# Kernel tuning notes

Measured on AMD Instinct MI355X. Metric: run time of the kernel, lower is better.

## Reference

```python
import jax, jax.numpy as jnp
import numpy as np

D, H, L, P, NQ, B, DFF = 256, 8, 4, 4, 900, 4, 1024
SHAPES = [(128, 128), (64, 64), (32, 32), (16, 16)]
S = sum(h * w for h, w in SHAPES)  # 21760
HD = D // H


def setup_inputs() -> dict:
    key = jax.random.key(0)
    ks = iter(jax.random.split(key, 32))
    r = lambda sh, s=1.0: jax.random.normal(next(ks), sh, jnp.float32) * s
    return dict(
        tgt=r((B, NQ, D)),
        query_pos=r((B, NQ, D)),
        reference_points=jax.random.uniform(next(ks), (B, NQ, L, 2), jnp.float32),
        memory=r((B, S, D)),
        in_proj_w=r((D, 3 * D), 0.02), in_proj_b=jnp.zeros(3 * D, jnp.float32),
        out_proj_w=r((D, D), 0.02), out_proj_b=jnp.zeros(D, jnp.float32),
        ln1_g=jnp.ones(D, jnp.float32), ln1_b=jnp.zeros(D, jnp.float32),
        ln2_g=jnp.ones(D, jnp.float32), ln2_b=jnp.zeros(D, jnp.float32),
        ln3_g=jnp.ones(D, jnp.float32), ln3_b=jnp.zeros(D, jnp.float32),
        vproj_w=r((D, D), 0.02), vproj_b=jnp.zeros(D, jnp.float32),
        off_w=r((D, H * L * P * 2), 0.02), off_b=r((H * L * P * 2,), 0.5),
        aw_w=r((D, H * L * P), 0.02), aw_b=jnp.zeros(H * L * P, jnp.float32),
        oproj_w=r((D, D), 0.02), oproj_b=jnp.zeros(D, jnp.float32),
        lin1_w=r((D, DFF), 0.02), lin1_b=jnp.zeros(DFF, jnp.float32),
        lin2_w=r((DFF, D), 0.02), lin2_b=jnp.zeros(D, jnp.float32),
        spatial_shapes=np.array(SHAPES, np.int32),
        mem_mask=jnp.zeros((B, S), bool),
    )


def _ln(x, g, b):
    m = jnp.mean(x, -1, keepdims=True)
    v = jnp.mean((x - m) ** 2, -1, keepdims=True)
    return (x - m) * jax.lax.rsqrt(v + 1e-5) * g + b


def reference(tgt, query_pos, reference_points, memory,
              in_proj_w, in_proj_b, out_proj_w, out_proj_b,
              ln1_g, ln1_b, ln2_g, ln2_b, ln3_g, ln3_b,
              vproj_w, vproj_b, off_w, off_b, aw_w, aw_b, oproj_w, oproj_b,
              lin1_w, lin1_b, lin2_w, lin2_b, spatial_shapes, mem_mask):
    shapes = np.asarray(spatial_shapes)  # static level shapes

    # ---- self attention (nn.MultiheadAttention, q=k=tgt+pos, v=tgt) ----
    qp = tgt + query_pos
    q = qp @ in_proj_w[:, :D] + in_proj_b[:D]
    k = qp @ in_proj_w[:, D:2 * D] + in_proj_b[D:2 * D]
    v = tgt @ in_proj_w[:, 2 * D:] + in_proj_b[2 * D:]
    split = lambda x: x.reshape(B, NQ, H, HD).transpose(0, 2, 1, 3)
    qh, kh, vh = split(q), split(k), split(v)
    att = jax.nn.softmax(jnp.einsum('bhqd,bhkd->bhqk', qh, kh) / np.sqrt(HD).astype(np.float32), -1)
    sa = jnp.einsum('bhqk,bhkd->bhqd', att, vh).transpose(0, 2, 1, 3).reshape(B, NQ, D)
    tgt = _ln(tgt + sa @ out_proj_w + out_proj_b, ln2_g, ln2_b)

    # ---- MSDeformAttn cross attention ----
    query = tgt + query_pos
    value = memory @ vproj_w + vproj_b
    value = jnp.where(mem_mask[..., None], 0.0, value).reshape(B, S, H, HD)
    off = (query @ off_w + off_b).reshape(B, NQ, H, L, P, 2)
    aw = jax.nn.softmax((query @ aw_w + aw_b).reshape(B, NQ, H, L * P), -1).reshape(B, NQ, H, L, P)
    # offset normalizer is (W_l, H_l)
    normalizer = jnp.stack([jnp.asarray(shapes[:, 1]), jnp.asarray(shapes[:, 0])], -1).astype(jnp.float32)
    loc = reference_points[:, :, None, :, None, :] + off / normalizer[None, None, None, :, None, :]

    acc = jnp.zeros((B, NQ, H, HD), tgt.dtype)
    start = 0
    bidx = jnp.arange(B)[:, None, None, None]
    hidx = jnp.arange(H)[None, None, :, None]
    for l in range(L):
        Hl, Wl = int(shapes[l, 0]), int(shapes[l, 1])
        vf = value[:, start:start + Hl * Wl]  # [B, Hl*Wl, H, HD]
        # grid_sample align_corners=False, zero padding: pixel = loc*size - 0.5
        x = loc[:, :, :, l, :, 0] * Wl - 0.5  # [B,NQ,H,P]
        y = loc[:, :, :, l, :, 1] * Hl - 0.5
        x0 = jnp.floor(x); y0 = jnp.floor(y)
        wx = x - x0; wy = y - y0
        x0i = x0.astype(jnp.int32); y0i = y0.astype(jnp.int32)

        def gather(xi, yi):
            valid = (xi >= 0) & (xi < Wl) & (yi >= 0) & (yi < Hl)
            idx = jnp.clip(yi, 0, Hl - 1) * Wl + jnp.clip(xi, 0, Wl - 1)
            g = vf[bidx, idx, hidx]  # [B,NQ,H,P,HD]
            return jnp.where(valid[..., None], g, 0.0)

        samp = (gather(x0i, y0i) * ((1 - wx) * (1 - wy))[..., None]
                + gather(x0i + 1, y0i) * (wx * (1 - wy))[..., None]
                + gather(x0i, y0i + 1) * ((1 - wx) * wy)[..., None]
                + gather(x0i + 1, y0i + 1) * (wx * wy)[..., None])
        acc = acc + (samp * aw[:, :, :, l, :, None]).sum(3)
        start += Hl * Wl

    ca = acc.reshape(B, NQ, D) @ oproj_w + oproj_b
    tgt = _ln(tgt + ca, ln1_g, ln1_b)

    # ---- FFN ----
    ff = jax.nn.relu(tgt @ lin1_w + lin1_b) @ lin2_w + lin2_b
    return _ln(tgt + ff, ln3_g, ln3_b)
```

## Files before the change

### kernel.cpp

```cpp
#include <hip/hip_runtime.h>
#include <hip/hip_bf16.h>

typedef __attribute__((ext_vector_type(8))) short bf16x8;
typedef __attribute__((ext_vector_type(4))) short bf16x4;
typedef __attribute__((ext_vector_type(4))) float f32x4;

#define DEV static __device__ __forceinline__

constexpr int Bc = 4, NQc = 900, Hc = 8, Sc = 21760;
constexpr int M1 = Bc * NQc;
constexpr int NQT = (NQc + 63) / 64;
constexpr int QT16 = (NQc + 15) / 16;

DEV short f2bf(float f) {
  union { __hip_bfloat16 h; short s; } u;
  u.h = __float2bfloat16(f);
  return u.s;
}
DEV float bf2f(short s) {
  union { short s; __hip_bfloat16 h; } u;
  u.s = s;
  return __bfloat162float(u.h);
}

DEV void pack_body(const float* W, short* Wt, int K, int N, int t) {
  int n = t % N;
  int k4 = (t / N) * 4;
  bf16x4 o;
  o[0] = f2bf(W[(size_t)(k4 + 0) * N + n]);
  o[1] = f2bf(W[(size_t)(k4 + 1) * N + n]);
  o[2] = f2bf(W[(size_t)(k4 + 2) * N + n]);
  o[3] = f2bf(W[(size_t)(k4 + 3) * N + n]);
  *(bf16x4*)&Wt[((size_t)(k4 >> 5) * N + n) * 32 + (k4 & 31)] = o;
}

__global__ __launch_bounds__(256) void pack_all_k(
    const float* w0, short* t0, const float* w1, short* t1,
    const float* w2, short* t2, const float* w3, short* t3,
    const float* w4, short* t4, const float* w5, short* t5) {
  int t = blockIdx.x * 256 + threadIdx.x;
  if (t < 49152) pack_body(w0, t0, 256, 768, t);
  else if (t < 65536) pack_body(w1, t1, 256, 256, t - 49152);
  else if (t < 81920) pack_body(w2, t2, 256, 256, t - 65536);
  else if (t < 98304) pack_body(w3, t3, 256, 256, t - 81920);
  else if (t < 163840) pack_body(w4, t4, 256, 1024, t - 98304);
  else pack_body(w5, t5, 1024, 256, t - 163840);
}

template <int MODE, int ACT, int MT>
__global__ __launch_bounds__(256) void gemmv_k(
    const float* __restrict__ A, const float* __restrict__ A2,
    const short* __restrict__ Wt, const float* __restrict__ bias,
    void* __restrict__ Cv, float* __restrict__ C2, int M, int N, int K,
    const unsigned char* __restrict__ rowmask, const float* __restrict__ g,
    const float* __restrict__ beta, const float* __restrict__ resid,
    const float* __restrict__ qpos, float* __restrict__ out2) {
  constexpr int IT = MT / 16;
  __shared__ short As[MT * 40];
  __shared__ short Ws[256 * 40];
  const int nb = N >> 8;
  const int mb = blockIdx.x / nb, bn = blockIdx.x - mb * nb;
  const int tid = threadIdx.x;
  const int lane = tid & 63, wave = tid >> 6;
  const int l16 = lane & 15, quad = lane >> 4;
  const int sr = (MT == 64) ? (tid >> 2) : (tid >> 3);
  const int sk = (MT == 64) ? ((tid & 3) * 8) : ((tid & 7) * 4);
  const int arow = mb * MT + sr;
  const bool aval = arow < M;
  const bool useA2 = (MODE == 2) ? (bn < 2) : (A2 != nullptr);
  const float* ap = A + (size_t)arow * K + sk;
  const float* ap2 = (A2 ? A2 : A) + (size_t)arow * K + sk;
  const short* wp = Wt + (size_t)(bn * 256 + tid) * 32;
  const size_t wstep = (size_t)N * 32;
  const int KT = K >> 5;

  f32x4 acc[IT][4] = {};
  float4 pa0[2] = {}, pa1[2] = {};
  bf16x8 pw[2][4];

  auto loadA = [&](int s, int it) {
    if (aval) {
      const float* p = ap + it * 32;
      pa0[s] = *(const float4*)p;
      if constexpr (MT == 64) pa1[s] = *(const float4*)(p + 4);
      if (useA2) {
        const float* p2 = ap2 + it * 32;
        float4 q0 = *(const float4*)p2;
        pa0[s].x += q0.x; pa0[s].y += q0.y; pa0[s].z += q0.z; pa0[s].w += q0.w;
        if constexpr (MT == 64) {
          float4 q1 = *(const float4*)(p2 + 4);
          pa1[s].x += q1.x; pa1[s].y += q1.y; pa1[s].z += q1.z; pa1[s].w += q1.w;
        }
      }
    }
  };
  auto loadW = [&](int s, int it) {
    const short* p = wp + (size_t)it * wstep;
    pw[s][0] = *(const bf16x8*)(p + 0);
    pw[s][1] = *(const bf16x8*)(p + 8);
    pw[s][2] = *(const bf16x8*)(p + 16);
    pw[s][3] = *(const bf16x8*)(p + 24);
  };
  auto stage = [&](int s) {
    if constexpr (MT == 64) {
      bf16x8 t;
      t[0] = f2bf(pa0[s].x); t[1] = f2bf(pa0[s].y); t[2] = f2bf(pa0[s].z); t[3] = f2bf(pa0[s].w);
      t[4] = f2bf(pa1[s].x); t[5] = f2bf(pa1[s].y); t[6] = f2bf(pa1[s].z); t[7] = f2bf(pa1[s].w);
      *(bf16x8*)&As[sr * 40 + sk] = t;
    } else {
      bf16x4 t;
      t[0] = f2bf(pa0[s].x); t[1] = f2bf(pa0[s].y); t[2] = f2bf(pa0[s].z); t[3] = f2bf(pa0[s].w);
      *(bf16x4*)&As[sr * 40 + sk] = t;
    }
    short* wd = &Ws[tid * 40];
    *(bf16x8*)(wd + 0) = pw[s][0];
    *(bf16x8*)(wd + 8) = pw[s][1];
    *(bf16x8*)(wd + 16) = pw[s][2];
    *(bf16x8*)(wd + 24) = pw[s][3];
  };
  auto compute = [&]() {
    bf16x8 af[IT], bfr[4];
#pragma unroll
    for (int i = 0; i < IT; i++)
      af[i] = *(const bf16x8*)&As[(i * 16 + l16) * 40 + quad * 8];
#pragma unroll
    for (int j = 0; j < 4; j++)
      bfr[j] = *(const bf16x8*)&Ws[(wave * 64 + j * 16 + l16) * 40 + quad * 8];
#pragma unroll
    for (int i = 0; i < IT; i++)
#pragma unroll
      for (int j = 0; j < 4; j++)
        acc[i][j] = __builtin_amdgcn_mfma_f32_16x16x32_bf16(af[i], bfr[j], acc[i][j], 0, 0, 0);
  };

  loadA(0, 0); loadW(0, 0);
  loadA(1, 1); loadW(1, 1);
  for (int it = 0; it < KT; it += 2) {
    stage(0);
    __syncthreads();
    if (it + 2 < KT) { loadA(0, it + 2); loadW(0, it + 2); }
    compute();
    __syncthreads();
    stage(1);
    __syncthreads();
    if (it + 3 < KT) { loadA(1, it + 3); loadW(1, it + 3); }
    compute();
    __syncthreads();
  }

  if constexpr (MODE == 2) {
    const bool isqk = (bn < 2);
    float* dst = isqk ? (float*)Cv : C2;
    const int stride = isqk ? 512 : 256;
    const int cb = isqk ? bn * 256 : 0;
#pragma unroll
    for (int i = 0; i < IT; i++)
#pragma unroll
      for (int j = 0; j < 4; j++) {
        const int cl = wave * 64 + j * 16 + l16;
        const float bb = bias[bn * 256 + cl];
#pragma unroll
        for (int r = 0; r < 4; r++) {
          const int m = mb * MT + i * 16 + quad * 4 + r;
          if (m < M) dst[(size_t)m * stride + cb + cl] = acc[i][j][r] + bb;
        }
      }
  } else if constexpr (MODE == 1) {
#pragma unroll
    for (int i = 0; i < IT; i++)
#pragma unroll
      for (int j = 0; j < 4; j++) {
        const int cl = wave * 64 + j * 16 + l16;
        const float bb = bias[cl];
#pragma unroll
        for (int r = 0; r < 4; r++) {
          const int m = mb * MT + i * 16 + quad * 4 + r;
          if (m < M) {
            float v = acc[i][j][r] + bb;
            if (rowmask[m]) v = 0.f;
            ((short*)Cv)[(size_t)m * 256 + cl] = f2bf(v);
          }
        }
      }
  } else if constexpr (MODE == 0) {
#pragma unroll
    for (int i = 0; i < IT; i++)
#pragma unroll
      for (int j = 0; j < 4; j++) {
        const int cl = wave * 64 + j * 16 + l16;
        const int col = bn * 256 + cl;
        const float bb = bias[col];
#pragma unroll
        for (int r = 0; r < 4; r++) {
          const int m = mb * MT + i * 16 + quad * 4 + r;
          if (m < M) {
            float v = acc[i][j][r] + bb;
            if (ACT == 1) v = fmaxf(v, 0.f);
            ((float*)Cv)[(size_t)m * N + col] = v;
          }
        }
      }
  } else {
#pragma unroll
    for (int j = 0; j < 4; j++) {
      const int cl = wave * 64 + j * 16 + l16;
      const float bb = bias[cl];
#pragma unroll
      for (int i = 0; i < IT; i++)
#pragma unroll
        for (int r = 0; r < 4; r++) {
          const int m = mb * MT + i * 16 + quad * 4 + r;
          const float rs = (m < M) ? resid[(size_t)m * 256 + cl] : 0.f;
          acc[i][j][r] += bb + rs;
        }
    }
    float2* pr = (float2*)As;
#pragma unroll
    for (int i = 0; i < IT; i++)
#pragma unroll
      for (int r = 0; r < 4; r++) {
        float s = 0.f, q = 0.f;
#pragma unroll
        for (int j = 0; j < 4; j++) {
          s += acc[i][j][r];
          q += acc[i][j][r] * acc[i][j][r];
        }
#pragma unroll
        for (int d = 1; d < 16; d <<= 1) {
          s += __shfl_xor(s, d);
          q += __shfl_xor(q, d);
        }
        if (l16 == 0) pr[(i * 16 + quad * 4 + r) * 4 + wave] = make_float2(s, q);
      }
    __syncthreads();
#pragma unroll
    for (int i = 0; i < IT; i++)
#pragma unroll
      for (int r = 0; r < 4; r++) {
        const int ml = i * 16 + quad * 4 + r;
        float2 p0 = pr[ml * 4 + 0], p1 = pr[ml * 4 + 1];
        float2 p2 = pr[ml * 4 + 2], p3 = pr[ml * 4 + 3];
        const float sum = p0.x + p1.x + p2.x + p3.x;
        const float sq = p0.y + p1.y + p2.y + p3.y;
        const float mean = sum * (1.f / 256.f);
        const float var = sq * (1.f / 256.f) - mean * mean;
        const float rstd = rsqrtf(var + 1e-5f);
        const int m = mb * MT + ml;
        if (m < M) {
#pragma unroll
          for (int j = 0; j < 4; j++) {
            const int cl = wave * 64 + j * 16 + l16;
            const float o = (acc[i][j][r] - mean) * rstd * g[cl] + beta[cl];
            ((float*)Cv)[(size_t)m * 256 + cl] = o;
            if (out2) out2[(size_t)m * 256 + cl] = o + qpos[(size_t)m * 256 + cl];
          }
        }
      }
  }
}

DEV void gemm32_body(const float* __restrict__ A, const float* __restrict__ W,
                     const float* __restrict__ bias, float* __restrict__ C,
                     int M, int N, int K, int bid) {
  __shared__ float Asf[16][64];
  __shared__ float Bsf[16][68];
  const int nb = N >> 6;
  const int bm = bid / nb, bn = bid % nb;
  const int tid = threadIdx.x;
  const int tm = tid >> 4, tn = tid & 15;
  float acc[4][4] = {};

  for (int k0 = 0; k0 < K; k0 += 16) {
    {
      const int m = tid >> 2, kk = (tid & 3) * 4;
      const int row = bm * 64 + m;
      float4 v = (row < M) ? *(const float4*)(A + (size_t)row * K + k0 + kk)
                           : make_float4(0.f, 0.f, 0.f, 0.f);
      Asf[kk + 0][m] = v.x; Asf[kk + 1][m] = v.y;
      Asf[kk + 2][m] = v.z; Asf[kk + 3][m] = v.w;
    }
    {
      const int kk = tid >> 4, n = (tid & 15) * 4;
      float4 v = *(const float4*)(W + (size_t)(k0 + kk) * N + bn * 64 + n);
      *(float4*)&Bsf[kk][n] = v;
    }
    __syncthreads();
#pragma unroll
    for (int kk = 0; kk < 16; kk++) {
      float a[4], b[4];
#pragma unroll
      for (int i = 0; i < 4; i++) a[i] = Asf[kk][tm * 4 + i];
#pragma unroll
      for (int j = 0; j < 4; j++) b[j] = Bsf[kk][tn * 4 + j];
#pragma unroll
      for (int i = 0; i < 4; i++)
#pragma unroll
        for (int j = 0; j < 4; j++) acc[i][j] = fmaf(a[i], b[j], acc[i][j]);
    }
    __syncthreads();
  }
#pragma unroll
  for (int i = 0; i < 4; i++) {
    const int row = bm * 64 + tm * 4 + i;
    if (row >= M) continue;
#pragma unroll
    for (int j = 0; j < 4; j++) {
      const int col = bn * 64 + tn * 4 + j;
      C[(size_t)row * N + col] = acc[i][j] + bias[col];
    }
  }
}

__global__ __launch_bounds__(256) void gemm32_offaw_k(
    const float* __restrict__ query, const float* __restrict__ off_w,
    const float* __restrict__ off_b, float* __restrict__ offb,
    const float* __restrict__ aw_w, const float* __restrict__ aw_b,
    float* __restrict__ awlin) {
  if (blockIdx.x < 228)
    gemm32_body(query, off_w, off_b, offb, M1, 256, 256, blockIdx.x);
  else
    gemm32_body(query, aw_w, aw_b, awlin, M1, 128, 256, blockIdx.x - 228);
}

__global__ __launch_bounds__(256) void attn_k(const float* __restrict__ qk,
                                              const float* __restrict__ vbuf,
                                              float* __restrict__ sa) {
  __shared__ short Vt[4][32 * 72];
  __shared__ short Pb[4][16 * 72];
  __shared__ float Om[4][16][32];
  __shared__ float Ml[4][16][2];
  const int bid = blockIdx.x;
  const int qt = bid % QT16, bh = bid / QT16;
  const int b = bh >> 3, h = bh & 7;
  const int tid = threadIdx.x, lane = tid & 63, wave = tid >> 6;
  const int l16 = lane & 15, quad = lane >> 4;

  const int q_local = qt * 16 + l16;
  const int qrow = b * NQc + min(q_local, NQc - 1);
  const float scale = 0.17677669529663687f;
  bf16x8 qf;
  {
    const float* qp = qk + (size_t)qrow * 512 + h * 32 + quad * 8;
    float4 v0 = *(const float4*)qp, v1 = *(const float4*)(qp + 4);
    qf[0] = f2bf(v0.x * scale); qf[1] = f2bf(v0.y * scale);
    qf[2] = f2bf(v0.z * scale); qf[3] = f2bf(v0.w * scale);
    qf[4] = f2bf(v1.x * scale); qf[5] = f2bf(v1.y * scale);
    qf[6] = f2bf(v1.z * scale); qf[7] = f2bf(v1.w * scale);
  }
  f32x4 o0 = {}, o1 = {};
  float mrun[4] = {-1e30f, -1e30f, -1e30f, -1e30f};
  float lrun[4] = {0.f, 0.f, 0.f, 0.f};

  short* vt = Vt[wave];
  short* pw = Pb[wave];
  const int vch = lane & 31, vkk = lane >> 5;

  for (int kt = wave; kt < NQT; kt += 4) {
    const int k0 = kt * 64;
#pragma unroll
    for (int i = 0; i < 32; i++) {
      const int key = k0 + 2 * i + vkk;
      const float v = (key < NQc) ? vbuf[(size_t)(b * NQc + key) * 256 + h * 32 + vch] : 0.f;
      vt[vch * 72 + 2 * i + vkk] = f2bf(v);
    }
    f32x4 s[4];
#pragma unroll
    for (int st = 0; st < 4; st++) {
      const int key = k0 + st * 16 + l16;
      const int krow = b * NQc + min(key, NQc - 1);
      const float* kp = qk + (size_t)krow * 512 + 256 + h * 32 + quad * 8;
      float4 v0 = *(const float4*)kp, v1 = *(const float4*)(kp + 4);
      bf16x8 kf;
      kf[0] = f2bf(v0.x); kf[1] = f2bf(v0.y); kf[2] = f2bf(v0.z); kf[3] = f2bf(v0.w);
      kf[4] = f2bf(v1.x); kf[5] = f2bf(v1.y); kf[6] = f2bf(v1.z); kf[7] = f2bf(v1.w);
      f32x4 z = {};
      s[st] = __builtin_amdgcn_mfma_f32_16x16x32_bf16(qf, kf, z, 0, 0, 0);
      if (key >= NQc) { s[st][0] = -1e30f; s[st][1] = -1e30f; s[st][2] = -1e30f; s[st][3] = -1e30f; }
    }
    float mnew[4], alpha[4];
#pragma unroll
    for (int r = 0; r < 4; r++) {
      float mx = fmaxf(fmaxf(s[0][r], s[1][r]), fmaxf(s[2][r], s[3][r]));
#pragma unroll
      for (int d = 1; d < 16; d <<= 1) mx = fmaxf(mx, __shfl_xor(mx, d));
      mnew[r] = fmaxf(mrun[r], mx);
      alpha[r] = __expf(mrun[r] - mnew[r]);
      mrun[r] = mnew[r];
    }
    float tsum[4] = {0.f, 0.f, 0.f, 0.f};
#pragma unroll
    for (int st = 0; st < 4; st++)
#pragma unroll
      for (int r = 0; r < 4; r++) {
        float p = __expf(s[st][r] - mnew[r]);
        s[st][r] = p;
        tsum[r] += p;
      }
#pragma unroll
    for (int r = 0; r < 4; r++) {
      float t = tsum[r];
#pragma unroll
      for (int d = 1; d < 16; d <<= 1) t += __shfl_xor(t, d);
      lrun[r] = lrun[r] * alpha[r] + t;
      o0[r] *= alpha[r];
      o1[r] *= alpha[r];
    }
#pragma unroll
    for (int st = 0; st < 4; st++)
#pragma unroll
      for (int r = 0; r < 4; r++)
        pw[(quad * 4 + r) * 72 + st * 16 + l16] = f2bf(s[st][r]);
#pragma unroll
    for (int c = 0; c < 2; c++) {
      bf16x8 pf = *(const bf16x8*)&pw[l16 * 72 + c * 32 + quad * 8];
      bf16x8 vf0 = *(const bf16x8*)&vt[l16 * 72 + c * 32 + quad * 8];
      bf16x8 vf1 = *(const bf16x8*)&vt[(16 + l16) * 72 + c * 32 + quad * 8];
      o0 = __builtin_amdgcn_mfma_f32_16x16x32_bf16(pf, vf0, o0, 0, 0, 0);
      o1 = __builtin_amdgcn_mfma_f32_16x16x32_bf16(pf, vf1, o1, 0, 0, 0);
    }
  }
#pragma unroll
  for (int r = 0; r < 4; r++) {
    Om[wave][quad * 4 + r][l16] = o0[r];
    Om[wave][quad * 4 + r][16 + l16] = o1[r];
  }
  if (l16 == 0) {
#pragma unroll
    for (int r = 0; r < 4; r++) {
      Ml[wave][quad * 4 + r][0] = mrun[r];
      Ml[wave][quad * 4 + r][1] = lrun[r];
    }
  }
  __syncthreads();
  {
    const int q = tid >> 4;
    const int c2 = (tid & 15) * 2;
    const float m0 = Ml[0][q][0], m1 = Ml[1][q][0];
    const float m2 = Ml[2][q][0], m3 = Ml[3][q][0];
    const float M = fmaxf(fmaxf(m0, m1), fmaxf(m2, m3));
    const float a0 = __expf(m0 - M), a1 = __expf(m1 - M);
    const float a2 = __expf(m2 - M), a3 = __expf(m3 - M);
    const float lsum = a0 * Ml[0][q][1] + a1 * Ml[1][q][1] +
                       a2 * Ml[2][q][1] + a3 * Ml[3][q][1];
    const float s0 = a0 * Om[0][q][c2] + a1 * Om[1][q][c2] +
                     a2 * Om[2][q][c2] + a3 * Om[3][q][c2];
    const float s1 = a0 * Om[0][q][c2 + 1] + a1 * Om[1][q][c2 + 1] +
                     a2 * Om[2][q][c2 + 1] + a3 * Om[3][q][c2 + 1];
    const int qg = qt * 16 + q;
    if (qg < NQc) {
      const float inv = 1.f / lsum;
      float* dst = sa + ((size_t)(b * NQc + qg) * 256 + h * 32 + c2);
      dst[0] = s0 * inv;
      dst[1] = s1 * inv;
    }
  }
}

__global__ __launch_bounds__(256) void sample_k(
    const float* __restrict__ awlin, const float* __restrict__ off,
    const float* __restrict__ refp, const short* __restrict__ value,
    float* __restrict__ accout) {
  const int wid = blockIdx.x * 4 + (threadIdx.x >> 6);
  const int lane = threadIdx.x & 63;
  const int bq = wid >> 3, h = wid & 7;
  const int b = bq / NQc;
  const int l16 = lane & 15;

  float wraw = awlin[(size_t)bq * 128 + h * 16 + l16];
  float mx = wraw;
#pragma unroll
  for (int d = 1; d < 16; d <<= 1) mx = fmaxf(mx, __shfl_xor(mx, d));
  float e = __expf(wraw - mx), ssum = e;
#pragma unroll
  for (int d = 1; d < 16; d <<= 1) ssum += __shfl_xor(ssum, d);
  const float wnorm = e / ssum;

  const int ch = lane & 31, sub = lane >> 5;
  float facc = 0.f;
#pragma unroll
  for (int it = 0; it < 8; it++) {
    const int pt = it * 2 + sub;
    const float w = __shfl(wnorm, pt);
    const int l = pt >> 2;
    const int W = 128 >> l;
    const int start = (l == 0) ? 0 : (l == 1) ? 16384 : (l == 2) ? 20480 : 21504;
    const float offx = off[(size_t)bq * 256 + h * 32 + pt * 2];
    const float offy = off[(size_t)bq * 256 + h * 32 + pt * 2 + 1];
    const float rx = refp[(size_t)bq * 8 + l * 2];
    const float ry = refp[(size_t)bq * 8 + l * 2 + 1];
    const float x = rx * (float)W + offx - 0.5f;
    const float y = ry * (float)W + offy - 0.5f;
    const float x0f = floorf(x), y0f = floorf(y);
    const float wx = x - x0f, wy = y - y0f;
    const int x0 = (int)x0f, y0 = (int)y0f;
    const short* vb = value + ((size_t)b * Sc + start) * 256 + h * 32 + ch;
#pragma unroll
    for (int c4 = 0; c4 < 4; c4++) {
      const int dx = c4 & 1, dy = c4 >> 1;
      const int xi = x0 + dx, yi = y0 + dy;
      const bool valid = (xi >= 0) && (xi < W) && (yi >= 0) && (yi < W);
      const int xc = min(max(xi, 0), W - 1);
      const int yc = min(max(yi, 0), W - 1);
      const float gvv = bf2f(vb[(size_t)(yc * W + xc) * 256]);
      const float ww = (dx ? wx : 1.f - wx) * (dy ? wy : 1.f - wy);
      facc += valid ? w * ww * gvv : 0.f;
    }
  }
  facc += __shfl_xor(facc, 32);
  if (lane < 32) accout[(size_t)bq * 256 + h * 32 + ch] = facc;
}

extern "C" void kernel_launch(void* const* d_in, const int* in_sizes, int n_in,
                              void* d_out, int out_size, void* d_ws,
                              size_t ws_size, hipStream_t stream) {
  const float* tgt = (const float*)d_in[0];
  const float* query_pos = (const float*)d_in[1];
  const float* refp = (const float*)d_in[2];
  const float* memory = (const float*)d_in[3];
  const float* in_proj_w = (const float*)d_in[4];
  const float* in_proj_b = (const float*)d_in[5];
  const float* out_proj_w = (const float*)d_in[6];
  const float* out_proj_b = (const float*)d_in[7];
  const float* ln1_g = (const float*)d_in[8];
  const float* ln1_b = (const float*)d_in[9];
  const float* ln2_g = (const float*)d_in[10];
  const float* ln2_b = (const float*)d_in[11];
  const float* ln3_g = (const float*)d_in[12];
  const float* ln3_b = (const float*)d_in[13];
  const float* vproj_w = (const float*)d_in[14];
  const float* vproj_b = (const float*)d_in[15];
  const float* off_w = (const float*)d_in[16];
  const float* off_b = (const float*)d_in[17];
  const float* aw_w = (const float*)d_in[18];
  const float* aw_b = (const float*)d_in[19];
  const float* oproj_w = (const float*)d_in[20];
  const float* oproj_b = (const float*)d_in[21];
  const float* lin1_w = (const float*)d_in[22];
  const float* lin1_b = (const float*)d_in[23];
  const float* lin2_w = (const float*)d_in[24];
  const float* lin2_b = (const float*)d_in[25];
  const unsigned char* mem_mask = (const unsigned char*)d_in[27];
  float* out = (float*)d_out;

  float* ws = (float*)d_ws;
  float* qkbuf = ws + 921600;
  float* vbuf = ws + 2764800;
  float* sa = ws + 3686400;
  float* tgt2 = ws + 5529600;
  float* query = ws + 6451200;
  float* offb = ws + 7372800;
  float* awlin = ws + 8294400;
  float* accb = ws + 8755200;
  float* tgt3 = ws + 9676800;
  float* ff1 = ws + 10598400;
  short* valueBf = (short*)(ws + 14284800);
  short* wbase = valueBf + 22282240;
  short* inT = wbase + 0;
  short* outT = wbase + 196608;
  short* vT = wbase + 262144;
  short* oT = wbase + 327680;
  short* lin1T = wbase + 393216;
  short* lin2T = wbase + 655360;

  pack_all_k<<<896, 256, 0, stream>>>(in_proj_w, inT, out_proj_w, outT,
                                      vproj_w, vT, oproj_w, oT,
                                      lin1_w, lin1T, lin2_w, lin2T);

  gemmv_k<2, 0, 32><<<113 * 3, 256, 0, stream>>>(
      tgt, query_pos, inT, in_proj_b, qkbuf, vbuf, M1, 768, 256,
      nullptr, nullptr, nullptr, nullptr, nullptr, nullptr);
  attn_k<<<Bc * Hc * QT16, 256, 0, stream>>>(qkbuf, vbuf, sa);
  gemmv_k<3, 0, 32><<<113, 256, 0, stream>>>(
      sa, nullptr, outT, out_proj_b, tgt2, nullptr, M1, 256, 256,
      nullptr, ln2_g, ln2_b, tgt, query_pos, query);
  gemmv_k<1, 0, 64><<<1360, 256, 0, stream>>>(
      memory, nullptr, vT, vproj_b, valueBf, nullptr, Bc * Sc, 256, 256,
      mem_mask, nullptr, nullptr, nullptr, nullptr, nullptr);
  gemm32_offaw_k<<<342, 256, 0, stream>>>(query, off_w, off_b, offb, aw_w, aw_b, awlin);
  sample_k<<<Bc * NQc * Hc / 4, 256, 0, stream>>>(awlin, offb, refp, valueBf, accb);
  gemmv_k<3, 0, 32><<<113, 256, 0, stream>>>(
      accb, nullptr, oT, oproj_b, tgt3, nullptr, M1, 256, 256,
      nullptr, ln1_g, ln1_b, tgt2, nullptr, nullptr);
  gemmv_k<0, 1, 64><<<57 * 4, 256, 0, stream>>>(
      tgt3, nullptr, lin1T, lin1_b, ff1, nullptr, M1, 1024, 256,
      nullptr, nullptr, nullptr, nullptr, nullptr, nullptr);
  gemmv_k<3, 0, 32><<<113, 256, 0, stream>>>(
      ff1, nullptr, lin2T, lin2_b, out, nullptr, M1, 256, 1024,
      nullptr, ln3_g, ln3_b, tgt3, nullptr, nullptr);
}
```

Measured before the change: 470.4 us.

## Emit bf16 head-major Q/K/V-transposed layouts from QKV GEMM; add 128-row value GEMM

```diff
diff --git a/kernel.cpp b/kernel.cpp
--- a/kernel.cpp
+++ b/kernel.cpp
@@ -11,6 +11,7 @@
 constexpr int M1 = Bc * NQc;
 constexpr int NQT = (NQc + 63) / 64;
 constexpr int QT16 = (NQc + 15) / 16;
+constexpr int QKo = Bc * Hc * 960 * 32;
 
 DEV short f2bf(float f) {
   union { __hip_bfloat16 h; short s; } u;
@@ -67,7 +68,7 @@
   const int sk = (MT == 64) ? ((tid & 3) * 8) : ((tid & 7) * 4);
   const int arow = mb * MT + sr;
   const bool aval = arow < M;
-  const bool useA2 = (MODE == 2) ? (bn < 2) : (A2 != nullptr);
+  const bool useA2 = (MODE == 4) ? (bn < 2) : (A2 != nullptr);
   const float* ap = A + (size_t)arow * K + sk;
   const float* ap2 = (A2 ? A2 : A) + (size_t)arow * K + sk;
   const short* wp = Wt + (size_t)(bn * 256 + tid) * 32;
@@ -148,37 +149,27 @@
     __syncthreads();
   }
 
-  if constexpr (MODE == 2) {
-    const bool isqk = (bn < 2);
-    float* dst = isqk ? (float*)Cv : C2;
-    const int stride = isqk ? 512 : 256;
-    const int cb = isqk ? bn * 256 : 0;
+  if constexpr (MODE == 4) {
+    short* base = (short*)Cv;
 #pragma unroll
     for (int i = 0; i < IT; i++)
 #pragma unroll
-      for (int j = 0; j < 4; j++) {
-        const int cl = wave * 64 + j * 16 + l16;
-        const float bb = bias[bn * 256 + cl];
-#pragma unroll
-        for (int r = 0; r < 4; r++) {
-          const int m = mb * MT + i * 16 + quad * 4 + r;
-          if (m < M) dst[(size_t)m * stride + cb + cl] = acc[i][j][r] + bb;
-        }
-      }
-  } else if constexpr (MODE == 1) {
-#pragma unroll
-    for (int i = 0; i < IT; i++)
-#pragma unroll
-      for (int j = 0; j < 4; j++) {
-        const int cl = wave * 64 + j * 16 + l16;
-        const float bb = bias[cl];
-#pragma unroll
-        for (int r = 0; r < 4; r++) {
-          const int m = mb * MT + i * 16 + quad * 4 + r;
-          if (m < M) {
-            float v = acc[i][j][r] + bb;
-            if (rowmask[m]) v = 0.f;
-            ((short*)Cv)[(size_t)m * 256 + cl] = f2bf(v);
+      for (int r = 0; r < 4; r++) {
+        const int m = mb * MT + i * 16 + quad * 4 + r;
+        if (m >= M) continue;
+        const int b = m / NQc, q = m - b * NQc;
+#pragma unroll
+        for (int j = 0; j < 4; j++) {
+          const int cl = wave * 64 + j * 16 + l16;
+          const float v = acc[i][j][r] + bias[bn * 256 + cl];
+          const int h = cl >> 5, ch = cl & 31;
+          if (bn == 0) {
+            base[((size_t)(b * 8 + h) * 960 + q) * 32 + ch] =
+                f2bf(v * 0.17677669529663687f);
+          } else if (bn == 1) {
+            base[QKo + ((size_t)(b * 8 + h) * 960 + q) * 32 + ch] = f2bf(v);
+          } else {
+            base[2 * QKo + ((((size_t)(b * 8 + h) * 15 + (q >> 6)) * 32 + ch) * 64 + (q & 63))] = f2bf(v);
           }
         }
       }
@@ -259,6 +250,90 @@
   }
 }
 
+__global__ __launch_bounds__(256) void gemm_val_k(
+    const float* __restrict__ A, const short* __restrict__ Wt,
+    const float* __restrict__ bias, short* __restrict__ Cv, int M,
+    const unsigned char* __restrict__ rowmask) {
+  __shared__ short As[128 * 40];
+  __shared__ short Ws[256 * 40];
+  const int mb = blockIdx.x;
+  const int tid = threadIdx.x;
+  const int lane = tid & 63, wave = tid >> 6;
+  const int l16 = lane & 15, quad = lane >> 4;
+  const int sr = tid >> 1, sk = (tid & 1) * 16;
+  const int arow = mb * 128 + sr;
+  const bool aval = arow < M;
+  const float* ap = A + (size_t)arow * 256 + sk;
+  const short* wp = Wt + (size_t)tid * 32;
+
+  f32x4 acc[8][4] = {};
+  float4 pa[4];
+  bf16x8 pwr[4];
+
+  auto loadA = [&](int it) {
+    if (aval) {
+#pragma unroll
+      for (int i = 0; i < 4; i++) pa[i] = *(const float4*)(ap + it * 32 + i * 4);
+    }
+  };
+  auto loadW = [&](int it) {
+    const short* p = wp + (size_t)it * (256 * 32);
+    pwr[0] = *(const bf16x8*)(p + 0);
+    pwr[1] = *(const bf16x8*)(p + 8);
+    pwr[2] = *(const bf16x8*)(p + 16);
+    pwr[3] = *(const bf16x8*)(p + 24);
+  };
+
+  loadA(0); loadW(0);
+  for (int it = 0; it < 8; ++it) {
+    {
+      bf16x8 t0, t1;
+      t0[0] = f2bf(pa[0].x); t0[1] = f2bf(pa[0].y); t0[2] = f2bf(pa[0].z); t0[3] = f2bf(pa[0].w);
+      t0[4] = f2bf(pa[1].x); t0[5] = f2bf(pa[1].y); t0[6] = f2bf(pa[1].z); t0[7] = f2bf(pa[1].w);
+      t1[0] = f2bf(pa[2].x); t1[1] = f2bf(pa[2].y); t1[2] = f2bf(pa[2].z); t1[3] = f2bf(pa[2].w);
+      t1[4] = f2bf(pa[3].x); t1[5] = f2bf(pa[3].y); t1[6] = f2bf(pa[3].z); t1[7] = f2bf(pa[3].w);
+      *(bf16x8*)&As[sr * 40 + sk] = t0;
+      *(bf16x8*)&As[sr * 40 + sk + 8] = t1;
+      short* wd = &Ws[tid * 40];
+      *(bf16x8*)(wd + 0) = pwr[0];
+      *(bf16x8*)(wd + 8) = pwr[1];
+      *(bf16x8*)(wd + 16) = pwr[2];
+      *(bf16x8*)(wd + 24) = pwr[3];
+    }
+    __syncthreads();
+    if (it + 1 < 8) { loadA(it + 1); loadW(it + 1); }
+    bf16x8 af[8], bfr[4];
+#pragma unroll
+    for (int i = 0; i < 8; i++)
+      af[i] = *(const bf16x8*)&As[(i * 16 + l16) * 40 + quad * 8];
+#pragma unroll
+    for (int j = 0; j < 4; j++)
+      bfr[j] = *(const bf16x8*)&Ws[(wave * 64 + j * 16 + l16) * 40 + quad * 8];
+#pragma unroll
+    for (int i = 0; i < 8; i++)
+#pragma unroll
+      for (int j = 0; j < 4; j++)
+        acc[i][j] = __builtin_amdgcn_mfma_f32_16x16x32_bf16(af[i], bfr[j], acc[i][j], 0, 0, 0);
+    __syncthreads();
+  }
+#pragma unroll
+  for (int i = 0; i < 8; i++)
+#pragma unroll
+    for (int j = 0; j < 4; j++) {
+      const int cl = wave * 64 + j * 16 + l16;
+      const float bb = bias[cl];
+#pragma unroll
+      for (int r = 0; r < 4; r++) {
+        const int m = mb * 128 + i * 16 + quad * 4 + r;
+        if (m < M) {
+          float v = acc[i][j][r] + bb;
+          if (rowmask[m]) v = 0.f;
+          Cv[(size_t)m * 256 + cl] = f2bf(v);
+        }
+      }
+    }
+}
+
 DEV void gemm32_body(const float* __restrict__ A, const float* __restrict__ W,
                      const float* __restrict__ bias, float* __restrict__ C,
                      int M, int N, int K, int bid) {
@@ -322,57 +397,35 @@
     gemm32_body(query, aw_w, aw_b, awlin, M1, 128, 256, blockIdx.x - 228);
 }
 
-__global__ __launch_bounds__(256) void attn_k(const float* __restrict__ qk,
-                                              const float* __restrict__ vbuf,
+__global__ __launch_bounds__(128) void attn_k(const short* __restrict__ qbf,
+                                              const short* __restrict__ kbf,
+                                              const short* __restrict__ vtbf,
                                               float* __restrict__ sa) {
-  __shared__ short Vt[4][32 * 72];
-  __shared__ short Pb[4][16 * 72];
-  __shared__ float Om[4][16][32];
-  __shared__ float Ml[4][16][2];
+  __shared__ short Pb[2][16 * 72];
+  __shared__ float Om[2][16][32];
+  __shared__ float Ml[2][16][2];
   const int bid = blockIdx.x;
   const int qt = bid % QT16, bh = bid / QT16;
-  const int b = bh >> 3, h = bh & 7;
   const int tid = threadIdx.x, lane = tid & 63, wave = tid >> 6;
   const int l16 = lane & 15, quad = lane >> 4;
 
-  const int q_local = qt * 16 + l16;
-  const int qrow = b * NQc + min(q_local, NQc - 1);
-  const float scale = 0.17677669529663687f;
-  bf16x8 qf;
-  {
-    const float* qp = qk + (size_t)qrow * 512 + h * 32 + quad * 8;
-    float4 v0 = *(const float4*)qp, v1 = *(const float4*)(qp + 4);
-    qf[0] = f2bf(v0.x * scale); qf[1] = f2bf(v0.y * scale);
-    qf[2] = f2bf(v0.z * scale); qf[3] = f2bf(v0.w * scale);
-    qf[4] = f2bf(v1.x * scale); qf[5] = f2bf(v1.y * scale);
-    qf[6] = f2bf(v1.z * scale); qf[7] = f2bf(v1.w * scale);
-  }
+  const int q_local = min(qt * 16 + l16, NQc - 1);
+  const bf16x8 qf = *(const bf16x8*)&qbf[((size_t)bh * 960 + q_local) * 32 + quad * 8];
+  const short* kb = kbf + (size_t)bh * 960 * 32;
+  const short* vb = vtbf + (size_t)bh * 15 * 32 * 64;
+
   f32x4 o0 = {}, o1 = {};
   float mrun[4] = {-1e30f, -1e30f, -1e30f, -1e30f};
   float lrun[4] = {0.f, 0.f, 0.f, 0.f};
-
-  short* vt = Vt[wave];
   short* pw = Pb[wave];
-  const int vch = lane & 31, vkk = lane >> 5;
-
-  for (int kt = wave; kt < NQT; kt += 4) {
+
+  for (int kt = wave; kt < NQT; kt += 2) {
     const int k0 = kt * 64;
-#pragma unroll
-    for (int i = 0; i < 32; i++) {
-      const int key = k0 + 2 * i + vkk;
-      const float v = (key < NQc) ? vbuf[(size_t)(b * NQc + key) * 256 + h * 32 + vch] : 0.f;
-      vt[vch * 72 + 2 * i + vkk] = f2bf(v);
-    }
     f32x4 s[4];
 #pragma unroll
     for (int st = 0; st < 4; st++) {
       const int key = k0 + st * 16 + l16;
-      const int krow = b * NQc + min(key, NQc - 1);
-      const float* kp = qk + (size_t)krow * 512 + 256 + h * 32 + quad * 8;
-      float4 v0 = *(const float4*)kp, v1 = *(const float4*)(kp + 4);
-      bf16x8 kf;
-      kf[0] = f2bf(v0.x); kf[1] = f2bf(v0.y); kf[2] = f2bf(v0.z); kf[3] = f2bf(v0.w);
-      kf[4] = f2bf(v1.x); kf[5] = f2bf(v1.y); kf[6] = f2bf(v1.z); kf[7] = f2bf(v1.w);
+      const bf16x8 kf = *(const bf16x8*)&kb[(size_t)key * 32 + quad * 8];
       f32x4 z = {};
       s[st] = __builtin_amdgcn_mfma_f32_16x16x32_bf16(qf, kf, z, 0, 0, 0);
       if (key >= NQc) { s[st][0] = -1e30f; s[st][1] = -1e30f; s[st][2] = -1e30f; s[st][3] = -1e30f; }
@@ -410,11 +463,12 @@
 #pragma unroll
       for (int r = 0; r < 4; r++)
         pw[(quad * 4 + r) * 72 + st * 16 + l16] = f2bf(s[st][r]);
+    const short* vt = vb + kt * (32 * 64);
 #pragma unroll
     for (int c = 0; c < 2; c++) {
       bf16x8 pf = *(const bf16x8*)&pw[l16 * 72 + c * 32 + quad * 8];
-      bf16x8 vf0 = *(const bf16x8*)&vt[l16 * 72 + c * 32 + quad * 8];
-      bf16x8 vf1 = *(const bf16x8*)&vt[(16 + l16) * 72 + c * 32 + quad * 8];
+      bf16x8 vf0 = *(const bf16x8*)&vt[(size_t)l16 * 64 + c * 32 + quad * 8];
+      bf16x8 vf1 = *(const bf16x8*)&vt[(size_t)(16 + l16) * 64 + c * 32 + quad * 8];
       o0 = __builtin_amdgcn_mfma_f32_16x16x32_bf16(pf, vf0, o0, 0, 0, 0);
       o1 = __builtin_amdgcn_mfma_f32_16x16x32_bf16(pf, vf1, o1, 0, 0, 0);
     }
@@ -433,25 +487,22 @@
   }
   __syncthreads();
   {
-    const int q = tid >> 4;
-    const int c2 = (tid & 15) * 2;
+    const int q = tid >> 3;
+    const int c4 = (tid & 7) * 4;
     const float m0 = Ml[0][q][0], m1 = Ml[1][q][0];
-    const float m2 = Ml[2][q][0], m3 = Ml[3][q][0];
-    const float M = fmaxf(fmaxf(m0, m1), fmaxf(m2, m3));
+    const float M = fmaxf(m0, m1);
     const float a0 = __expf(m0 - M), a1 = __expf(m1 - M);
-    const float a2 = __expf(m2 - M), a3 = __expf(m3 - M);
-    const float lsum = a0 * Ml[0][q][1] + a1 * Ml[1][q][1] +
-                       a2 * Ml[2][q][1] + a3 * Ml[3][q][1];
-    const float s0 = a0 * Om[0][q][c2] + a1 * Om[1][q][c2] +
-                     a2 * Om[2][q][c2] + a3 * Om[3][q][c2];
-    const float s1 = a0 * Om[0][q][c2 + 1] + a1 * Om[1][q][c2 + 1] +
-                     a2 * Om[2][q][c2 + 1] + a3 * Om[3][q][c2 + 1];
+    const float lsum = a0 * Ml[0][q][1] + a1 * Ml[1][q][1];
     const int qg = qt * 16 + q;
     if (qg < NQc) {
       const float inv = 1.f / lsum;
-      float* dst = sa + ((size_t)(b * NQc + qg) * 256 + h * 32 + c2);
-      dst[0] = s0 * inv;
-      dst[1] = s1 * inv;
+      float4 o;
+      o.x = (a0 * Om[0][q][c4 + 0] + a1 * Om[1][q][c4 + 0]) * inv;
+      o.y = (a0 * Om[0][q][c4 + 1] + a1 * Om[1][q][c4 + 1]) * inv;
+      o.z = (a0 * Om[0][q][c4 + 2] + a1 * Om[1][q][c4 + 2]) * inv;
+      o.w = (a0 * Om[0][q][c4 + 3] + a1 * Om[1][q][c4 + 3]) * inv;
+      const int b = bh >> 3, h = bh & 7;
+      *(float4*)&sa[(size_t)(b * NQc + qg) * 256 + h * 32 + c4] = o;
     }
   }
 }
@@ -493,7 +544,7 @@
     const float x0f = floorf(x), y0f = floorf(y);
     const float wx = x - x0f, wy = y - y0f;
     const int x0 = (int)x0f, y0 = (int)y0f;
-    const short* vb = value + ((size_t)b * Sc + start) * 256 + h * 32 + ch;
+    const short* vbp = value + ((size_t)b * Sc + start) * 256 + h * 32 + ch;
 #pragma unroll
     for (int c4 = 0; c4 < 4; c4++) {
       const int dx = c4 & 1, dy = c4 >> 1;
@@ -501,7 +552,7 @@
       const bool valid = (xi >= 0) && (xi < W) && (yi >= 0) && (yi < W);
       const int xc = min(max(xi, 0), W - 1);
       const int yc = min(max(yi, 0), W - 1);
-      const float gvv = bf2f(vb[(size_t)(yc * W + xc) * 256]);
+      const float gvv = bf2f(vbp[(size_t)(yc * W + xc) * 256]);
       const float ww = (dx ? wx : 1.f - wx) * (dy ? wy : 1.f - wy);
       facc += valid ? w * ww * gvv : 0.f;
     }
@@ -543,8 +594,7 @@
   float* out = (float*)d_out;
 
   float* ws = (float*)d_ws;
-  float* qkbuf = ws + 921600;
-  float* vbuf = ws + 2764800;
+  short* qbf = (short*)(ws + 921600);
   float* sa = ws + 3686400;
   float* tgt2 = ws + 5529600;
   float* query = ws + 6451200;
@@ -566,16 +616,14 @@
                                       vproj_w, vT, oproj_w, oT,
                                       lin1_w, lin1T, lin2_w, lin2T);
 
-  gemmv_k<2, 0, 32><<<113 * 3, 256, 0, stream>>>(
-      tgt, query_pos, inT, in_proj_b, qkbuf, vbuf, M1, 768, 256,
+  gemmv_k<4, 0, 32><<<113 * 3, 256, 0, stream>>>(
+      tgt, query_pos, inT, in_proj_b, qbf, nullptr, M1, 768, 256,
       nullptr, nullptr, nullptr, nullptr, nullptr, nullptr);
-  attn_k<<<Bc * Hc * QT16, 256, 0, stream>>>(qkbuf, vbuf, sa);
+  attn_k<<<Bc * Hc * QT16, 128, 0, stream>>>(qbf, qbf + QKo, qbf + 2 * QKo, sa);
   gemmv_k<3, 0, 32><<<113, 256, 0, stream>>>(
       sa, nullptr, outT, out_proj_b, tgt2, nullptr, M1, 256, 256,
       nullptr, ln2_g, ln2_b, tgt, query_pos, query);
-  gemmv_k<1, 0, 64><<<1360, 256, 0, stream>>>(
-      memory, nullptr, vT, vproj_b, valueBf, nullptr, Bc * Sc, 256, 256,
-      mem_mask, nullptr, nullptr, nullptr, nullptr, nullptr);
+  gemm_val_k<<<680, 256, 0, stream>>>(memory, vT, vproj_b, valueBf, Bc * Sc, mem_mask);
   gemm32_offaw_k<<<342, 256, 0, stream>>>(query, off_w, off_b, offb, aw_w, aw_b, awlin);
   sample_k<<<Bc * NQc * Hc / 4, 256, 0, stream>>>(awlin, offb, refp, valueBf, accb);
   gemmv_k<3, 0, 32><<<113, 256, 0, stream>>>(
```

Result: faster. 427.3 us (-9.2%).
